# Optimization experiments

Hardware: AMD Instinct MI355X
Metric: run time of the kernel (lower is better)

The kernel has to match this reference:

```python
import jax, jax.numpy as jnp
import numpy as np

N_NODES = 50000
EMBED = 64
N_EDGES = 1250000
N_USERS = 25000
BATCH, K = 1024, 100


def setup_inputs() -> dict:
    key = jax.random.key(0)
    ks = jax.random.split(key, 8)
    stdv = 1.0 / np.sqrt(EMBED)
    emb = jax.random.uniform(ks[0], (N_NODES, EMBED), jnp.float32, -stdv, stdv)
    # nn.Linear default init: U(-1/sqrt(fan_in), 1/sqrt(fan_in))
    lim = 1.0 / np.sqrt(EMBED)
    W0 = jax.random.uniform(ks[1], (EMBED, EMBED), jnp.float32, -lim, lim)
    b0 = jax.random.uniform(ks[2], (EMBED,), jnp.float32, -lim, lim)
    W1 = jax.random.uniform(ks[3], (EMBED, EMBED), jnp.float32, -lim, lim)
    b1 = jax.random.uniform(ks[4], (EMBED,), jnp.float32, -lim, lim)
    src = jax.random.randint(ks[5], (N_EDGES,), 0, N_NODES, jnp.int32)
    dst = jax.random.randint(ks[6], (N_EDGES,), 0, N_NODES, jnp.int32)
    user_index = jax.random.randint(ks[7], (BATCH, K), 0, N_USERS, jnp.int32)
    item_index = jax.random.randint(jax.random.fold_in(key, 99), (BATCH, K), 0, N_NODES, jnp.int32)
    return {"embeddings": emb, "W0": W0, "b0": b0, "W1": W1, "b1": b1,
            "src": src, "dst": dst, "user_index": user_index, "item_index": item_index}


def _mean_aggregate(h, src, dst):
    # copy_src gather + mailbox mean: mean of src features over incoming edges per dst
    msg_sum = jax.ops.segment_sum(h[src], dst, num_segments=N_NODES)  # [N, D]
    deg = jax.ops.segment_sum(jnp.ones((src.shape[0],), h.dtype), dst, num_segments=N_NODES)
    return msg_sum / jnp.maximum(deg, 1.0)[:, None]


def reference(embeddings, W0, b0, W1, b1, src, dst, user_index, item_index):
    h = embeddings
    for W, b in ((W0, b0), (W1, b1)):
        agg = _mean_aggregate(h, src, dst)          # [N, D] mean mailbox
        h = jnp.tanh(agg @ W.T + b)                  # NodeUpdate: Linear + Tanh
    user = h[user_index]                             # [B, K, D]
    item = h[item_index]                             # [B, K, D]
    score = jnp.sum(user * item, axis=2)             # [B, K]
    return score
```

## Files before the change

### kernel.cpp

```cpp
#include <hip/hip_runtime.h>

#define N_NODES 50000
#define N_EDGES 1250000
#define EMBED 64
#define N_PAIRS (1024 * 100)
#define BSHIFT 7
#define BSIZE 128
#define NBUCK 391
#define CB 153
#define LDS_CAP 4096

__global__ __launch_bounds__(1024) void hist_kernel(const int* __restrict__ dst,
                                                    int* __restrict__ counts) {
    __shared__ int hl[NBUCK];
    int t = threadIdx.x, b = blockIdx.x;
    for (int i = t; i < NBUCK; i += 1024) hl[i] = 0;
    __syncthreads();
    #pragma unroll
    for (int rep = 0; rep < 2; ++rep) {
        int i4 = b * 2048 + rep * 1024 + t;
        if (i4 < N_EDGES / 4) {
            int4 d = ((const int4*)dst)[i4];
            atomicAdd(&hl[d.x >> BSHIFT], 1);
            atomicAdd(&hl[d.y >> BSHIFT], 1);
            atomicAdd(&hl[d.z >> BSHIFT], 1);
            atomicAdd(&hl[d.w >> BSHIFT], 1);
        }
    }
    __syncthreads();
    for (int i = t; i < NBUCK; i += 1024) counts[b * NBUCK + i] = hl[i];
}

__global__ __launch_bounds__(512) void prep_kernel(const int* __restrict__ counts,
                                                   int* __restrict__ offs,
                                                   int* __restrict__ base) {
    __shared__ int ws[8];
    int t = threadIdx.x, lane = t & 63, wid = t >> 6;
    int tot = 0;
    if (t < NBUCK)
        for (int b = 0; b < CB; ++b) tot += counts[b * NBUCK + t];
    int incl = tot;
    #pragma unroll
    for (int off = 1; off < 64; off <<= 1) {
        int o = __shfl_up(incl, off);
        if (lane >= off) incl += o;
    }
    if (lane == 63) ws[wid] = incl;
    __syncthreads();
    if (t < 8) {
        int x = ws[t];
        #pragma unroll
        for (int off = 1; off < 8; off <<= 1) {
            int o = __shfl_up(x, off);
            if (t >= off) x += o;
        }
        ws[t] = x;
    }
    __syncthreads();
    int ex = ((wid > 0) ? ws[wid - 1] : 0) + incl - tot;
    if (t < NBUCK) base[t] = ex;
    if (t == 0) base[NBUCK] = N_EDGES;
    if (t < NBUCK) {
        int run = ex;
        for (int b = 0; b < CB; ++b) {
            offs[b * NBUCK + t] = run;
            run += counts[b * NBUCK + t];
        }
    }
}

__global__ __launch_bounds__(1024) void scatter_kernel(const int* __restrict__ src,
                                                       const int* __restrict__ dst,
                                                       const int* __restrict__ offs,
                                                       unsigned int* __restrict__ pairs) {
    __shared__ int cur[NBUCK];
    int t = threadIdx.x, b = blockIdx.x;
    for (int i = t; i < NBUCK; i += 1024) cur[i] = offs[b * NBUCK + i];
    __syncthreads();
    #pragma unroll
    for (int rep = 0; rep < 2; ++rep) {
        int i4 = b * 2048 + rep * 1024 + t;
        if (i4 < N_EDGES / 4) {
            int4 s4 = ((const int4*)src)[i4];
            int4 d4 = ((const int4*)dst)[i4];
            int p;
            p = atomicAdd(&cur[d4.x >> BSHIFT], 1);
            pairs[p] = ((unsigned)(d4.x & (BSIZE - 1)) << 16) | (unsigned)s4.x;
            p = atomicAdd(&cur[d4.y >> BSHIFT], 1);
            pairs[p] = ((unsigned)(d4.y & (BSIZE - 1)) << 16) | (unsigned)s4.y;
            p = atomicAdd(&cur[d4.z >> BSHIFT], 1);
            pairs[p] = ((unsigned)(d4.z & (BSIZE - 1)) << 16) | (unsigned)s4.z;
            p = atomicAdd(&cur[d4.w >> BSHIFT], 1);
            pairs[p] = ((unsigned)(d4.w & (BSIZE - 1)) << 16) | (unsigned)s4.w;
        }
    }
}

__global__ __launch_bounds__(256) void bucketsort_kernel(const unsigned int* __restrict__ pairs,
                                                         const int* __restrict__ base,
                                                         int* __restrict__ row,
                                                         int* __restrict__ col) {
    __shared__ unsigned ebuf[LDS_CAP];
    __shared__ int staged[LDS_CAP];
    __shared__ int hist[BSIZE];
    __shared__ int cur[BSIZE];
    __shared__ int wtot;
    int k = blockIdx.x, t = threadIdx.x;
    int lane = t & 63, wid = t >> 6;
    int nstart = k * BSIZE;
    int nodes = min(BSIZE, N_NODES - nstart);
    int estart = base[k], eend = base[k + 1];
    int cnt = eend - estart;
    if (t < BSIZE) hist[t] = 0;
    __syncthreads();
    if (cnt <= LDS_CAP) {
        for (int i = t; i < cnt; i += 256) {
            unsigned w = pairs[estart + i];
            ebuf[i] = w;
            atomicAdd(&hist[w >> 16], 1);
        }
        __syncthreads();
        if (t < BSIZE) {
            int v = hist[t];
            int incl = v;
            #pragma unroll
            for (int off = 1; off < 64; off <<= 1) {
                int o = __shfl_up(incl, off);
                if (lane >= off) incl += o;
            }
            if (t == 63) wtot = incl;
            __syncthreads();
            int ex = incl - v + ((wid == 1) ? wtot : 0);
            cur[t] = ex;
            if (t < nodes) row[nstart + t] = estart + ex;
        } else {
            __syncthreads();
        }
        if (k == NBUCK - 1 && t == 0) row[N_NODES] = N_EDGES;
        __syncthreads();
        for (int i = t; i < cnt; i += 256) {
            unsigned w = ebuf[i];
            int pos = atomicAdd(&cur[w >> 16], 1);
            staged[pos] = (int)(w & 0xFFFFu);
        }
        __syncthreads();
        for (int i = t; i < cnt; i += 256) col[estart + i] = staged[i];
    } else {
        for (int i = t; i < cnt; i += 256)
            atomicAdd(&hist[pairs[estart + i] >> 16], 1);
        __syncthreads();
        if (t < BSIZE) {
            int v = hist[t];
            int incl = v;
            #pragma unroll
            for (int off = 1; off < 64; off <<= 1) {
                int o = __shfl_up(incl, off);
                if (lane >= off) incl += o;
            }
            if (t == 63) wtot = incl;
            __syncthreads();
            int ex = incl - v + ((wid == 1) ? wtot : 0);
            cur[t] = ex;
            if (t < nodes) row[nstart + t] = estart + ex;
        } else {
            __syncthreads();
        }
        if (k == NBUCK - 1 && t == 0) row[N_NODES] = N_EDGES;
        __syncthreads();
        for (int i = t; i < cnt; i += 256) {
            unsigned w = pairs[estart + i];
            int pos = atomicAdd(&cur[w >> 16], 1);
            col[estart + pos] = (int)(w & 0xFFFFu);
        }
    }
}

__global__ __launch_bounds__(256) void gemv_kernel(const float* __restrict__ h,
                                                   const float* __restrict__ W,
                                                   float* __restrict__ g) {
    __shared__ float hL[64][64];
    __shared__ float Wl[64][65];
    int t = threadIdx.x;
    int nstart = blockIdx.x * 64;
    int lane = t & 63, wid = t >> 6;
    for (int i = t; i < 4096; i += 256) Wl[i & 63][i >> 6] = W[i];
    int nrem = min(64, N_NODES - nstart);
    for (int i = t; i < nrem * 16; i += 256)
        ((float4*)hL)[i] = ((const float4*)(h + (size_t)nstart * EMBED))[i];
    __syncthreads();
    for (int n = wid; n < nrem; n += 4) {
        float x = 0.f;
        #pragma unroll
        for (int d = 0; d < 64; ++d)
            x += hL[n][d] * Wl[d][lane];
        g[(size_t)(nstart + n) * EMBED + lane] = x;
    }
}

__global__ __launch_bounds__(256) void agg_kernel(const float* __restrict__ g,
                                                  const float* __restrict__ bias,
                                                  const int* __restrict__ row,
                                                  const int* __restrict__ col,
                                                  float* __restrict__ hout) {
    int t = threadIdx.x;
    int wid = t >> 6, lane = t & 63;
    int node = blockIdx.x * 4 + wid;
    int gg = lane >> 4, d16 = lane & 15;
    int start = row[node], end = row[node + 1];
    float4 bb = ((const float4*)bias)[d16];
    float4 acc = {0.f, 0.f, 0.f, 0.f};
    for (int e = start; e < end; e += 16) {
        int e0 = e + gg, e1 = e + 4 + gg, e2 = e + 8 + gg, e3 = e + 12 + gg;
        bool k0 = e0 < end, k1 = e1 < end, k2 = e2 < end, k3 = e3 < end;
        int s0 = k0 ? col[e0] : 0;
        int s1 = k1 ? col[e1] : 0;
        int s2 = k2 ? col[e2] : 0;
        int s3 = k3 ? col[e3] : 0;
        float4 v0 = {0,0,0,0}, v1 = {0,0,0,0}, v2 = {0,0,0,0}, v3 = {0,0,0,0};
        if (k0) v0 = ((const float4*)(g + (size_t)s0 * EMBED))[d16];
        if (k1) v1 = ((const float4*)(g + (size_t)s1 * EMBED))[d16];
        if (k2) v2 = ((const float4*)(g + (size_t)s2 * EMBED))[d16];
        if (k3) v3 = ((const float4*)(g + (size_t)s3 * EMBED))[d16];
        acc.x += (v0.x + v1.x) + (v2.x + v3.x);
        acc.y += (v0.y + v1.y) + (v2.y + v3.y);
        acc.z += (v0.z + v1.z) + (v2.z + v3.z);
        acc.w += (v0.w + v1.w) + (v2.w + v3.w);
    }
    #pragma unroll
    for (int off = 16; off < 64; off <<= 1) {
        acc.x += __shfl_xor(acc.x, off);
        acc.y += __shfl_xor(acc.y, off);
        acc.z += __shfl_xor(acc.z, off);
        acc.w += __shfl_xor(acc.w, off);
    }
    int dg = end - start;
    float inv = (dg > 0) ? 1.0f / (float)dg : 0.f;
    if (gg == 0) {
        float4 o;
        o.x = tanhf(acc.x * inv + bb.x);
        o.y = tanhf(acc.y * inv + bb.y);
        o.z = tanhf(acc.z * inv + bb.z);
        o.w = tanhf(acc.w * inv + bb.w);
        ((float4*)(hout + (size_t)node * EMBED))[d16] = o;
    }
}

__global__ __launch_bounds__(256) void score_kernel(const float* __restrict__ h,
                                                    const int* __restrict__ ui,
                                                    const int* __restrict__ ii,
                                                    float* __restrict__ out) {
    int t = threadIdx.x;
    int idx = blockIdx.x * 16 + (t >> 4);
    int d16 = t & 15;
    int u = ui[idx];
    int v = ii[idx];
    float4 a = ((const float4*)(h + (size_t)u * EMBED))[d16];
    float4 b = ((const float4*)(h + (size_t)v * EMBED))[d16];
    float p = a.x * b.x + a.y * b.y + a.z * b.z + a.w * b.w;
    #pragma unroll
    for (int off = 8; off > 0; off >>= 1)
        p += __shfl_xor(p, off);
    if (d16 == 0) out[idx] = p;
}

extern "C" void kernel_launch(void* const* d_in, const int* in_sizes, int n_in,
                              void* d_out, int out_size, void* d_ws, size_t ws_size,
                              hipStream_t stream) {
    const float* emb = (const float*)d_in[0];
    const float* W0  = (const float*)d_in[1];
    const float* b0  = (const float*)d_in[2];
    const float* W1  = (const float*)d_in[3];
    const float* b1  = (const float*)d_in[4];
    const int* src   = (const int*)d_in[5];
    const int* dst   = (const int*)d_in[6];
    const int* ui    = (const int*)d_in[7];
    const int* ii    = (const int*)d_in[8];
    float* out = (float*)d_out;

    char* p = (char*)d_ws;
    auto alloc = [&](size_t bytes) {
        char* r = p;
        p += (bytes + 255) & ~(size_t)255;
        return r;
    };
    int* counts     = (int*)alloc(sizeof(int) * NBUCK * CB);
    int* offs       = (int*)alloc(sizeof(int) * NBUCK * CB);
    int* base       = (int*)alloc(sizeof(int) * (NBUCK + 1));
    int* row        = (int*)alloc(sizeof(int) * (N_NODES + 1));
    unsigned* pairs = (unsigned*)alloc(sizeof(unsigned) * N_EDGES);
    int* col        = (int*)alloc(sizeof(int) * N_EDGES);
    float* gbuf     = (float*)alloc(sizeof(float) * N_NODES * EMBED);
    float* hbuf     = (float*)alloc(sizeof(float) * N_NODES * EMBED);

    hist_kernel<<<CB, 1024, 0, stream>>>(dst, counts);
    prep_kernel<<<1, 512, 0, stream>>>(counts, offs, base);
    scatter_kernel<<<CB, 1024, 0, stream>>>(src, dst, offs, pairs);
    bucketsort_kernel<<<NBUCK, 256, 0, stream>>>(pairs, base, row, col);
    gemv_kernel<<<(N_NODES + 63) / 64, 256, 0, stream>>>(emb, W0, gbuf);
    agg_kernel<<<N_NODES / 4, 256, 0, stream>>>(gbuf, b0, row, col, hbuf);
    gemv_kernel<<<(N_NODES + 63) / 64, 256, 0, stream>>>(hbuf, W1, gbuf);
    agg_kernel<<<N_NODES / 4, 256, 0, stream>>>(gbuf, b1, row, col, hbuf);
    score_kernel<<<N_PAIRS / 16, 256, 0, stream>>>(hbuf, ui, ii, out);
}
```

Before: 249.6 us.

## Store intermediate node features in bf16 to halve gather traffic

Switches the transformed-feature buffer and hidden-state buffer from fp32 to bf16 storage, with fp32 accumulation. Adds a bf16-input gemv variant and converts on load in the aggregation and score kernels. The aggregation loop is also restructured to process 32 edges per iteration with per-edge predication. This targets the random-gather bandwidth of 1.25M edge reads per layer, at the cost of reduced precision in intermediate features.

```diff
diff --git a/kernel.cpp b/kernel.cpp
--- a/kernel.cpp
+++ b/kernel.cpp
@@ -9,6 +9,15 @@
 #define NBUCK 391
 #define CB 153
 #define LDS_CAP 4096
+
+__device__ inline float bf2f(unsigned short u) {
+    return __uint_as_float(((unsigned)u) << 16);
+}
+__device__ inline unsigned short f2bf(float x) {
+    unsigned u = __float_as_uint(x);
+    u += 0x7FFF + ((u >> 16) & 1);
+    return (unsigned short)(u >> 16);
+}
 
 __global__ __launch_bounds__(1024) void hist_kernel(const int* __restrict__ dst,
                                                     int* __restrict__ counts) {
@@ -175,9 +184,9 @@
     }
 }
 
-__global__ __launch_bounds__(256) void gemv_kernel(const float* __restrict__ h,
-                                                   const float* __restrict__ W,
-                                                   float* __restrict__ g) {
+__global__ __launch_bounds__(256) void gemv_f32_kernel(const float* __restrict__ h,
+                                                       const float* __restrict__ W,
+                                                       unsigned short* __restrict__ g) {
     __shared__ float hL[64][64];
     __shared__ float Wl[64][65];
     int t = threadIdx.x;
@@ -193,15 +202,43 @@
         #pragma unroll
         for (int d = 0; d < 64; ++d)
             x += hL[n][d] * Wl[d][lane];
-        g[(size_t)(nstart + n) * EMBED + lane] = x;
-    }
-}
-
-__global__ __launch_bounds__(256) void agg_kernel(const float* __restrict__ g,
+        g[(size_t)(nstart + n) * EMBED + lane] = f2bf(x);
+    }
+}
+
+__global__ __launch_bounds__(256) void gemv_bf16_kernel(const unsigned short* __restrict__ h,
+                                                        const float* __restrict__ W,
+                                                        unsigned short* __restrict__ g) {
+    __shared__ float hL[64][64];
+    __shared__ float Wl[64][65];
+    int t = threadIdx.x;
+    int nstart = blockIdx.x * 64;
+    int lane = t & 63, wid = t >> 6;
+    for (int i = t; i < 4096; i += 256) Wl[i & 63][i >> 6] = W[i];
+    int nrem = min(64, N_NODES - nstart);
+    for (int i = t; i < nrem * 16; i += 256) {
+        ushort4 v = ((const ushort4*)(h + (size_t)nstart * EMBED))[i];
+        int r = i >> 4, c = (i & 15) * 4;
+        hL[r][c + 0] = bf2f(v.x);
+        hL[r][c + 1] = bf2f(v.y);
+        hL[r][c + 2] = bf2f(v.z);
+        hL[r][c + 3] = bf2f(v.w);
+    }
+    __syncthreads();
+    for (int n = wid; n < nrem; n += 4) {
+        float x = 0.f;
+        #pragma unroll
+        for (int d = 0; d < 64; ++d)
+            x += hL[n][d] * Wl[d][lane];
+        g[(size_t)(nstart + n) * EMBED + lane] = f2bf(x);
+    }
+}
+
+__global__ __launch_bounds__(256) void agg_kernel(const unsigned short* __restrict__ g,
                                                   const float* __restrict__ bias,
                                                   const int* __restrict__ row,
                                                   const int* __restrict__ col,
-                                                  float* __restrict__ hout) {
+                                                  unsigned short* __restrict__ hout) {
     int t = threadIdx.x;
     int wid = t >> 6, lane = t & 63;
     int node = blockIdx.x * 4 + wid;
@@ -209,22 +246,19 @@
     int start = row[node], end = row[node + 1];
     float4 bb = ((const float4*)bias)[d16];
     float4 acc = {0.f, 0.f, 0.f, 0.f};
-    for (int e = start; e < end; e += 16) {
-        int e0 = e + gg, e1 = e + 4 + gg, e2 = e + 8 + gg, e3 = e + 12 + gg;
-        bool k0 = e0 < end, k1 = e1 < end, k2 = e2 < end, k3 = e3 < end;
-        int s0 = k0 ? col[e0] : 0;
-        int s1 = k1 ? col[e1] : 0;
-        int s2 = k2 ? col[e2] : 0;
-        int s3 = k3 ? col[e3] : 0;
-        float4 v0 = {0,0,0,0}, v1 = {0,0,0,0}, v2 = {0,0,0,0}, v3 = {0,0,0,0};
-        if (k0) v0 = ((const float4*)(g + (size_t)s0 * EMBED))[d16];
-        if (k1) v1 = ((const float4*)(g + (size_t)s1 * EMBED))[d16];
-        if (k2) v2 = ((const float4*)(g + (size_t)s2 * EMBED))[d16];
-        if (k3) v3 = ((const float4*)(g + (size_t)s3 * EMBED))[d16];
-        acc.x += (v0.x + v1.x) + (v2.x + v3.x);
-        acc.y += (v0.y + v1.y) + (v2.y + v3.y);
-        acc.z += (v0.z + v1.z) + (v2.z + v3.z);
-        acc.w += (v0.w + v1.w) + (v2.w + v3.w);
+    for (int e = start; e < end; e += 32) {
+        #pragma unroll
+        for (int k = 0; k < 8; ++k) {
+            int ee = e + 4 * k + gg;
+            if (ee < end) {
+                int s = col[ee];
+                ushort4 v = ((const ushort4*)(g + (size_t)s * EMBED))[d16];
+                acc.x += bf2f(v.x);
+                acc.y += bf2f(v.y);
+                acc.z += bf2f(v.z);
+                acc.w += bf2f(v.w);
+            }
+        }
     }
     #pragma unroll
     for (int off = 16; off < 64; off <<= 1) {
@@ -236,16 +270,16 @@
     int dg = end - start;
     float inv = (dg > 0) ? 1.0f / (float)dg : 0.f;
     if (gg == 0) {
-        float4 o;
-        o.x = tanhf(acc.x * inv + bb.x);
-        o.y = tanhf(acc.y * inv + bb.y);
-        o.z = tanhf(acc.z * inv + bb.z);
-        o.w = tanhf(acc.w * inv + bb.w);
-        ((float4*)(hout + (size_t)node * EMBED))[d16] = o;
-    }
-}
-
-__global__ __launch_bounds__(256) void score_kernel(const float* __restrict__ h,
+        ushort4 o;
+        o.x = f2bf(tanhf(acc.x * inv + bb.x));
+        o.y = f2bf(tanhf(acc.y * inv + bb.y));
+        o.z = f2bf(tanhf(acc.z * inv + bb.z));
+        o.w = f2bf(tanhf(acc.w * inv + bb.w));
+        ((ushort4*)(hout + (size_t)node * EMBED))[d16] = o;
+    }
+}
+
+__global__ __launch_bounds__(256) void score_kernel(const unsigned short* __restrict__ h,
                                                     const int* __restrict__ ui,
                                                     const int* __restrict__ ii,
                                                     float* __restrict__ out) {
@@ -254,9 +288,10 @@
     int d16 = t & 15;
     int u = ui[idx];
     int v = ii[idx];
-    float4 a = ((const float4*)(h + (size_t)u * EMBED))[d16];
-    float4 b = ((const float4*)(h + (size_t)v * EMBED))[d16];
-    float p = a.x * b.x + a.y * b.y + a.z * b.z + a.w * b.w;
+    ushort4 a4 = ((const ushort4*)(h + (size_t)u * EMBED))[d16];
+    ushort4 b4 = ((const ushort4*)(h + (size_t)v * EMBED))[d16];
+    float p = bf2f(a4.x) * bf2f(b4.x) + bf2f(a4.y) * bf2f(b4.y) +
+              bf2f(a4.z) * bf2f(b4.z) + bf2f(a4.w) * bf2f(b4.w);
     #pragma unroll
     for (int off = 8; off > 0; off >>= 1)
         p += __shfl_xor(p, off);
@@ -283,22 +318,22 @@
         p += (bytes + 255) & ~(size_t)255;
         return r;
     };
-    int* counts     = (int*)alloc(sizeof(int) * NBUCK * CB);
-    int* offs       = (int*)alloc(sizeof(int) * NBUCK * CB);
-    int* base       = (int*)alloc(sizeof(int) * (NBUCK + 1));
-    int* row        = (int*)alloc(sizeof(int) * (N_NODES + 1));
-    unsigned* pairs = (unsigned*)alloc(sizeof(unsigned) * N_EDGES);
-    int* col        = (int*)alloc(sizeof(int) * N_EDGES);
-    float* gbuf     = (float*)alloc(sizeof(float) * N_NODES * EMBED);
-    float* hbuf     = (float*)alloc(sizeof(float) * N_NODES * EMBED);
+    int* counts          = (int*)alloc(sizeof(int) * NBUCK * CB);
+    int* offs            = (int*)alloc(sizeof(int) * NBUCK * CB);
+    int* base            = (int*)alloc(sizeof(int) * (NBUCK + 1));
+    int* row             = (int*)alloc(sizeof(int) * (N_NODES + 1));
+    unsigned* pairs      = (unsigned*)alloc(sizeof(unsigned) * N_EDGES);
+    int* col             = (int*)alloc(sizeof(int) * N_EDGES);
+    unsigned short* gbuf = (unsigned short*)alloc(sizeof(unsigned short) * N_NODES * EMBED);
+    unsigned short* hbuf = (unsigned short*)alloc(sizeof(unsigned short) * N_NODES * EMBED);
 
     hist_kernel<<<CB, 1024, 0, stream>>>(dst, counts);
     prep_kernel<<<1, 512, 0, stream>>>(counts, offs, base);
     scatter_kernel<<<CB, 1024, 0, stream>>>(src, dst, offs, pairs);
     bucketsort_kernel<<<NBUCK, 256, 0, stream>>>(pairs, base, row, col);
-    gemv_kernel<<<(N_NODES + 63) / 64, 256, 0, stream>>>(emb, W0, gbuf);
+    gemv_f32_kernel<<<(N_NODES + 63) / 64, 256, 0, stream>>>(emb, W0, gbuf);
     agg_kernel<<<N_NODES / 4, 256, 0, stream>>>(gbuf, b0, row, col, hbuf);
-    gemv_kernel<<<(N_NODES + 63) / 64, 256, 0, stream>>>(hbuf, W1, gbuf);
+    gemv_bf16_kernel<<<(N_NODES + 63) / 64, 256, 0, stream>>>(hbuf, W1, gbuf);
     agg_kernel<<<N_NODES / 4, 256, 0, stream>>>(gbuf, b1, row, col, hbuf);
     score_kernel<<<N_PAIRS / 16, 256, 0, stream>>>(hbuf, ui, ii, out);
 }
```

Result: no change. 252.4 us (+1.1%).
